# Optimization experiments

Measured on AMD Instinct MI355X. Metric: run time of the kernel, lower is better.

## Reference

```python
import jax, jax.numpy as jnp
import numpy as np

D_MODEL = 256
N_HEAD = 8
HEAD_DIM = D_MODEL // N_HEAD
N_TOTAL = 24576
B, T = 64, 512


def setup_inputs() -> dict:
    key = jax.random.key(0)
    ks = jax.random.split(key, 12)
    s = 1.0 / np.sqrt(D_MODEL)
    return {
        "x": jax.random.normal(ks[0], (N_TOTAL, D_MODEL), jnp.float32),
        "Wq": jax.random.uniform(ks[1], (D_MODEL, D_MODEL), jnp.float32, -s, s),
        "bq": jax.random.uniform(ks[2], (D_MODEL,), jnp.float32, -s, s),
        "Wk": jax.random.uniform(ks[3], (D_MODEL, D_MODEL), jnp.float32, -s, s),
        "bk": jax.random.uniform(ks[4], (D_MODEL,), jnp.float32, -s, s),
        "Wv": jax.random.uniform(ks[5], (D_MODEL, D_MODEL), jnp.float32, -s, s),
        "bv": jax.random.uniform(ks[6], (D_MODEL,), jnp.float32, -s, s),
        "Wp": jax.random.uniform(ks[7], (D_MODEL, D_MODEL), jnp.float32, -s, s),
        "bp": jax.random.uniform(ks[8], (D_MODEL,), jnp.float32, -s, s),
        "padpack_index": jax.random.randint(ks[9], (B, T), 0, N_TOTAL, jnp.int64 if jax.config.jax_enable_x64 else jnp.int32),
        "padpack_batch": jax.random.randint(ks[10], (B, T), 0, B, jnp.int32),
        "padpack_inverse_index": jax.random.randint(ks[11], (N_TOTAL,), 0, B * T, jnp.int64 if jax.config.jax_enable_x64 else jnp.int32),
    }


def reference(x, Wq, bq, Wk, bk, Wv, bv, Wp, bp, padpack_index, padpack_batch, padpack_inverse_index):
    # gather ragged tokens into packed [B, T, C]
    xp = x[padpack_index]
    # mask: True where packed slots share the same segment id (matches
    # original masked_fill(batch_i == batch_j, -1e9))
    mask = padpack_batch[:, :, None] == padpack_batch[:, None, :]  # [B,T,T]
    # QKV projections (torch Linear: x @ W.T + b), split heads
    def heads(w, b):
        h = xp @ w.T + b
        return h.reshape(B, T, N_HEAD, HEAD_DIM).transpose(0, 2, 1, 3)  # [B,H,T,D]
    q, k, v = heads(Wq, bq), heads(Wk, bk), heads(Wv, bv)
    att = jnp.einsum("bhtd,bhsd->bhts", q, k) * (1.0 / np.sqrt(HEAD_DIM))
    att = jnp.where(mask[:, None], jnp.float32(-1e9), att)
    att = jax.nn.softmax(att, axis=-1)
    y = jnp.einsum("bhts,bhsd->bhtd", att, v)  # [B,H,T,D]
    y = y.transpose(0, 2, 1, 3).reshape(B, T, D_MODEL)
    y = y @ Wp.T + bp
    # scatter back to ragged layout
    return y.reshape(B * T, D_MODEL)[padpack_inverse_index]
```

## Files before the change

kernel.cpp:

```cpp
#include <hip/hip_runtime.h>


typedef __attribute__((ext_vector_type(8))) short short8;
typedef __attribute__((ext_vector_type(4))) float f32x4;

#define N_TOTAL 24576
#define B_ 64
#define T_ 512
#define M_TOK 32768
#define DM 256
#define NH 8
#define HD 32

#define QSCALE 0.25503463f

__device__ __forceinline__ unsigned short f2bf(float f) {
  unsigned int u = __float_as_uint(f);
  u += 0x7fffu + ((u >> 16) & 1u);
  return (unsigned short)(u >> 16);
}

__global__ __launch_bounds__(256) void pack_kernel(
    const float* __restrict__ x, const float* __restrict__ Wq,
    const float* __restrict__ Wk, const float* __restrict__ Wv,
    const float* __restrict__ Wp, const float* __restrict__ bq,
    const float* __restrict__ bk, const float* __restrict__ bv,
    const int* __restrict__ idx,
    short* __restrict__ XP, short* __restrict__ WCAT, short* __restrict__ WPb,
    float* __restrict__ BCAT) {
  int gid = blockIdx.x * 256 + threadIdx.x;
  if (gid < 768)
    BCAT[gid] = (gid < 256) ? bq[gid] : (gid < 512 ? bk[gid - 256] : bv[gid - 512]);
  const float* src;
  short* dst;
  if (gid < 1048576) {
    int row = gid >> 5, seg = gid & 31;
    src = x + (size_t)idx[row] * DM + seg * 8;
    dst = XP + (size_t)gid * 8;
  } else if (gid < 1073152) {
    int u = gid - 1048576;
    int f = u >> 5, seg = u & 31;
    const float* W = (f < 256) ? Wq : ((f < 512) ? Wk : Wv);
    src = W + (size_t)(f & 255) * DM + seg * 8;
    dst = WCAT + (size_t)u * 8;
  } else {
    int u = gid - 1073152;
    src = Wp + (size_t)u * 8;
    dst = WPb + (size_t)u * 8;
  }
  const float4* s4 = (const float4*)src;
  float4 a = s4[0], b = s4[1];
  short8 o;
  o[0] = (short)f2bf(a.x); o[1] = (short)f2bf(a.y);
  o[2] = (short)f2bf(a.z); o[3] = (short)f2bf(a.w);
  o[4] = (short)f2bf(b.x); o[5] = (short)f2bf(b.y);
  o[6] = (short)f2bf(b.z); o[7] = (short)f2bf(b.w);
  *(short8*)dst = o;
}

__global__ __launch_bounds__(256) void qkv_gemm(
    const short* __restrict__ XP, const short* __restrict__ WCAT,
    const float* __restrict__ BCAT,
    unsigned short* __restrict__ Qb, unsigned short* __restrict__ Kb,
    unsigned short* __restrict__ Vt) {
  __shared__ __align__(16) short As[128 * 40];
  __shared__ __align__(16) short Bs[128 * 40];
  int tid = threadIdx.x;
  int lane = tid & 63, w = tid >> 6;
  int i = lane & 15, q = lane >> 4;
  int m0 = blockIdx.x * 128, n0 = blockIdx.y * 128;
  int wm = (w & 1) * 64, wn = (w >> 1) * 64;

  f32x4 zf = {0.f, 0.f, 0.f, 0.f};
  f32x4 acc[4][4];
#pragma unroll
  for (int mt = 0; mt < 4; mt++)
#pragma unroll
    for (int nt = 0; nt < 4; nt++) acc[mt][nt] = zf;

  for (int k0 = 0; k0 < 256; k0 += 32) {
#pragma unroll
    for (int p = 0; p < 2; ++p) {
      int u = tid + p * 256;
      int row = u >> 2, seg = u & 3;
      *(short8*)&As[row * 40 + seg * 8] =
          *(const short8*)&XP[(size_t)(m0 + row) * DM + k0 + seg * 8];
      *(short8*)&Bs[row * 40 + seg * 8] =
          *(const short8*)&WCAT[(size_t)(n0 + row) * DM + k0 + seg * 8];
    }
    __syncthreads();
    short8 a[4], bfr[4];
#pragma unroll
    for (int mt = 0; mt < 4; mt++)
      a[mt] = *(short8*)&As[(wm + mt * 16 + i) * 40 + q * 8];
#pragma unroll
    for (int nt = 0; nt < 4; nt++)
      bfr[nt] = *(short8*)&Bs[(wn + nt * 16 + i) * 40 + q * 8];
#pragma unroll
    for (int mt = 0; mt < 4; mt++)
#pragma unroll
      for (int nt = 0; nt < 4; nt++)
        acc[mt][nt] = __builtin_amdgcn_mfma_f32_16x16x32_bf16(a[mt], bfr[nt], acc[mt][nt], 0, 0, 0);
    __syncthreads();
  }

#pragma unroll
  for (int nt = 0; nt < 4; nt++) {
    int f = n0 + wn + nt * 16 + i;
    float bias = BCAT[f];
    int which = f >> 8;
    int fw = f & 255;
    int hh = fw >> 5, dd = fw & 31;
#pragma unroll
    for (int mt = 0; mt < 4; mt++) {
#pragma unroll
      for (int r = 0; r < 4; r++) {
        int token = m0 + wm + mt * 16 + q * 4 + r;
        int bb = token >> 9, tt = token & 511;
        int bh = bb * NH + hh;
        float val = acc[mt][nt][r] + bias;
        if (which == 0)
          Qb[((size_t)bh * T_ + tt) * HD + dd] = f2bf(val * QSCALE);
        else if (which == 1)
          Kb[((size_t)bh * T_ + tt) * HD + dd] = f2bf(val);
        else
          Vt[((size_t)bh * HD + dd) * T_ + tt] = f2bf(val);
      }
    }
  }
}

__global__ __launch_bounds__(256) void attn_kernel(
    const short* __restrict__ Qb, const short* __restrict__ Kb,
    const short* __restrict__ Vt, const int* __restrict__ batch,
    unsigned short* __restrict__ Y) {
  __shared__ __align__(16) short pscr[4][64 * 40];
  __shared__ int sbat[T_];
  int tid = threadIdx.x, w = tid >> 6, lane = tid & 63;
  int i = lane & 15, q = lane >> 4;
  int bx = blockIdx.x;
  int half = bx >> 9, bh = bx & 511;
  int b = bh >> 3, h = bh & 7;
  int t0 = half * 256 + w * 64;

  *(int2*)&sbat[tid * 2] = *(const int2*)&batch[b * T_ + tid * 2];
  __syncthreads();

  const short* Kbase = Kb + (size_t)bh * T_ * HD;
  const short* Vbase = Vt + (size_t)bh * HD * T_;
  short* pw = &pscr[w][0];

  short8 qf[4];
  unsigned int btpk[4];
#pragma unroll
  for (int mt = 0; mt < 4; mt++) {
    qf[mt] = *(const short8*)&Kbase[((size_t)(t0 + mt * 16 + i) - (size_t)T_ * HD * 0) * HD + q * 8];
  }
#pragma unroll
  for (int mt = 0; mt < 4; mt++)
    qf[mt] = *(const short8*)&Qb[((size_t)bh * T_ + t0 + mt * 16 + i) * HD + q * 8];
#pragma unroll
  for (int mt = 0; mt < 4; mt++) {
    int4 t4 = *(int4*)&sbat[t0 + mt * 16 + q * 4];
    btpk[mt] = (unsigned)t4.x | ((unsigned)t4.y << 8) | ((unsigned)t4.z << 16) |
               ((unsigned)t4.w << 24);
  }

  unsigned short ob = (i == 0) ? (unsigned short)0x3F80 : (unsigned short)0;
  short8 ones = {(short)ob, (short)ob, (short)ob, (short)ob,
                 (short)ob, (short)ob, (short)ob, (short)ob};

  f32x4 zf = {0.f, 0.f, 0.f, 0.f};
  f32x4 o[4][2], lacc[4];
#pragma unroll
  for (int mt = 0; mt < 4; mt++) {
    o[mt][0] = zf; o[mt][1] = zf; lacc[mt] = zf;
  }

  for (int s0 = 0; s0 < T_; s0 += 32) {
    short8 k0f = *(const short8*)&Kbase[(s0 + i) * HD + q * 8];
    short8 k1f = *(const short8*)&Kbase[(s0 + 16 + i) * HD + q * 8];
    short8 v0f = *(const short8*)&Vbase[(size_t)i * T_ + s0 + q * 8];
    short8 v1f = *(const short8*)&Vbase[(size_t)(16 + i) * T_ + s0 + q * 8];
    int bs0 = sbat[s0 + i];
    int bs1 = sbat[s0 + 16 + i];
#pragma unroll
    for (int mt = 0; mt < 4; mt++) {
      f32x4 st0 = __builtin_amdgcn_mfma_f32_16x16x32_bf16(qf[mt], k0f, zf, 0, 0, 0);
      f32x4 st1 = __builtin_amdgcn_mfma_f32_16x16x32_bf16(qf[mt], k1f, zf, 0, 0, 0);
#pragma unroll
      for (int r = 0; r < 4; r++) {
        int btv = (int)((btpk[mt] >> (8 * r)) & 0xffu);
        float e0 = __builtin_amdgcn_exp2f(st0[r]);
        float e1 = __builtin_amdgcn_exp2f(st1[r]);
        unsigned short p0 =
            (btv == bs0) ? (unsigned short)0 : (unsigned short)(__float_as_uint(e0) >> 16);
        unsigned short p1 =
            (btv == bs1) ? (unsigned short)0 : (unsigned short)(__float_as_uint(e1) >> 16);
        pw[(mt * 16 + q * 4 + r) * 40 + i] = (short)p0;
        pw[(mt * 16 + q * 4 + r) * 40 + 16 + i] = (short)p1;
      }
    }
#pragma unroll
    for (int mt = 0; mt < 4; mt++) {
      short8 pa = *(short8*)&pw[(mt * 16 + i) * 40 + q * 8];
      o[mt][0] = __builtin_amdgcn_mfma_f32_16x16x32_bf16(pa, v0f, o[mt][0], 0, 0, 0);
      o[mt][1] = __builtin_amdgcn_mfma_f32_16x16x32_bf16(pa, v1f, o[mt][1], 0, 0, 0);
      lacc[mt] = __builtin_amdgcn_mfma_f32_16x16x32_bf16(pa, ones, lacc[mt], 0, 0, 0);
    }
  }

#pragma unroll
  for (int mt = 0; mt < 4; mt++) {
#pragma unroll
    for (int r = 0; r < 4; r++) {
      float lv = __shfl(lacc[mt][r], lane & 48, 64);
      float inv = __builtin_amdgcn_rcpf(lv);
      size_t yb = ((size_t)b * T_ + t0 + mt * 16 + q * 4 + r) * DM + h * HD;
      Y[yb + i] = f2bf(o[mt][0][r] * inv);
      Y[yb + 16 + i] = f2bf(o[mt][1][r] * inv);
    }
  }
}

__global__ __launch_bounds__(256) void out_gemm(
    const short* __restrict__ Y, const short* __restrict__ WPb,
    const float* __restrict__ bp, const int* __restrict__ inv,
    float* __restrict__ out) {
  __shared__ __align__(16) short As[128 * 40];
  __shared__ __align__(16) short Bs[128 * 40];
  int tid = threadIdx.x;
  int lane = tid & 63, w = tid >> 6;
  int i = lane & 15, q = lane >> 4;
  int m0 = blockIdx.x * 128, n0 = blockIdx.y * 128;
  int wm = (w & 1) * 64, wn = (w >> 1) * 64;

  int iv0 = inv[m0 + (tid >> 2)];
  int iv1 = inv[m0 + (tid >> 2) + 64];

  f32x4 zf = {0.f, 0.f, 0.f, 0.f};
  f32x4 acc[4][4];
#pragma unroll
  for (int mt = 0; mt < 4; mt++)
#pragma unroll
    for (int nt = 0; nt < 4; nt++) acc[mt][nt] = zf;

  for (int k0 = 0; k0 < 256; k0 += 32) {
#pragma unroll
    for (int p = 0; p < 2; ++p) {
      int u = tid + p * 256;
      int row = u >> 2, seg = u & 3;
      int iv = p ? iv1 : iv0;
      *(short8*)&As[row * 40 + seg * 8] =
          *(const short8*)&Y[(size_t)iv * DM + k0 + seg * 8];
      *(short8*)&Bs[row * 40 + seg * 8] =
          *(const short8*)&WPb[(size_t)(n0 + row) * DM + k0 + seg * 8];
    }
    __syncthreads();
    short8 a[4], bfr[4];
#pragma unroll
    for (int mt = 0; mt < 4; mt++)
      a[mt] = *(short8*)&As[(wm + mt * 16 + i) * 40 + q * 8];
#pragma unroll
    for (int nt = 0; nt < 4; nt++)
      bfr[nt] = *(short8*)&Bs[(wn + nt * 16 + i) * 40 + q * 8];
#pragma unroll
    for (int mt = 0; mt < 4; mt++)
#pragma unroll
      for (int nt = 0; nt < 4; nt++)
        acc[mt][nt] = __builtin_amdgcn_mfma_f32_16x16x32_bf16(a[mt], bfr[nt], acc[mt][nt], 0, 0, 0);
    __syncthreads();
  }

#pragma unroll
  for (int nt = 0; nt < 4; nt++) {
    int f = n0 + wn + nt * 16 + i;
    float bias = bp[f];
#pragma unroll
    for (int mt = 0; mt < 4; mt++) {
#pragma unroll
      for (int r = 0; r < 4; r++) {
        int row = m0 + wm + mt * 16 + q * 4 + r;
        out[(size_t)row * DM + f] = acc[mt][nt][r] + bias;
      }
    }
  }
}

extern "C" void kernel_launch(void* const* d_in, const int* in_sizes, int n_in,
                              void* d_out, int out_size, void* d_ws, size_t ws_size,
                              hipStream_t stream) {
  const float* x = (const float*)d_in[0];
  const float* Wq = (const float*)d_in[1];
  const float* bq = (const float*)d_in[2];
  const float* Wk = (const float*)d_in[3];
  const float* bk = (const float*)d_in[4];
  const float* Wv = (const float*)d_in[5];
  const float* bv = (const float*)d_in[6];
  const float* Wp = (const float*)d_in[7];
  const float* bp = (const float*)d_in[8];
  const int* idx = (const int*)d_in[9];
  const int* batch = (const int*)d_in[10];
  const int* inv = (const int*)d_in[11];
  float* out = (float*)d_out;

  char* ws = (char*)d_ws;
  short* XP = (short*)(ws + 0);
  short* WCAT = (short*)(ws + 16777216);
  short* WPb = (short*)(ws + 17170432);
  float* BCAT = (float*)(ws + 17301504);
  unsigned short* Qb = (unsigned short*)(ws + 17304576);
  unsigned short* Kb = (unsigned short*)(ws + 34081792);
  unsigned short* Vt = (unsigned short*)(ws + 50859008);
  unsigned short* Yb = (unsigned short*)(ws + 67636224);

  pack_kernel<<<4224, 256, 0, stream>>>(x, Wq, Wk, Wv, Wp, bq, bk, bv, idx,
                                        XP, WCAT, WPb, BCAT);
  qkv_gemm<<<dim3(256, 6), 256, 0, stream>>>(XP, WCAT, BCAT, Qb, Kb, Vt);
  attn_kernel<<<1024, 256, 0, stream>>>((const short*)Qb, (const short*)Kb,
                                        (const short*)Vt, batch, Yb);
  out_gemm<<<dim3(192, 2), 256, 0, stream>>>((const short*)Yb, WPb, bp, inv, out);
}
```

Before: 195.0 us.

## Pipeline GEMM tile loads with triple-buffered direct global-to-LDS copies

Both the QKV and output GEMMs now stage A and B tiles straight from global memory into LDS with global_load_lds, using three buffers and a prefetch distance of two k-steps. This replaces the register round-trip and the double __syncthreads per iteration with explicit waitcnt plus barrier, so loads overlap the MFMA work. The LDS layout drops the padding in favour of an XOR swizzle to avoid bank conflicts. A redundant K load in attention is also removed. The cost is more LDS per block, which may lower occupancy, and correctness depends on the hand-tuned vmcnt values.

```diff
diff --git a/kernel.cpp b/kernel.cpp
--- a/kernel.cpp
+++ b/kernel.cpp
@@ -18,6 +18,12 @@
   unsigned int u = __float_as_uint(f);
   u += 0x7fffu + ((u >> 16) & 1u);
   return (unsigned short)(u >> 16);
+}
+
+__device__ __forceinline__ void gl_lds16(const void* g, void* l) {
+  __builtin_amdgcn_global_load_lds(
+      (const __attribute__((address_space(1))) unsigned int*)g,
+      (__attribute__((address_space(3))) unsigned int*)l, 16, 0, 0);
 }
 
 __global__ __launch_bounds__(256) void pack_kernel(
@@ -63,13 +69,13 @@
     const float* __restrict__ BCAT,
     unsigned short* __restrict__ Qb, unsigned short* __restrict__ Kb,
     unsigned short* __restrict__ Vt) {
-  __shared__ __align__(16) short As[128 * 40];
-  __shared__ __align__(16) short Bs[128 * 40];
+  __shared__ __align__(16) char smem[3 * 16384];
   int tid = threadIdx.x;
   int lane = tid & 63, w = tid >> 6;
   int i = lane & 15, q = lane >> 4;
   int m0 = blockIdx.x * 128, n0 = blockIdx.y * 128;
   int wm = (w & 1) * 64, wn = (w >> 1) * 64;
+  int csa = q ^ ((i >> 1) & 3);
 
   f32x4 zf = {0.f, 0.f, 0.f, 0.f};
   f32x4 acc[4][4];
@@ -78,30 +84,42 @@
 #pragma unroll
     for (int nt = 0; nt < 4; nt++) acc[mt][nt] = zf;
 
-  for (int k0 = 0; k0 < 256; k0 += 32) {
-#pragma unroll
-    for (int p = 0; p < 2; ++p) {
-      int u = tid + p * 256;
-      int row = u >> 2, seg = u & 3;
-      *(short8*)&As[row * 40 + seg * 8] =
-          *(const short8*)&XP[(size_t)(m0 + row) * DM + k0 + seg * 8];
-      *(short8*)&Bs[row * 40 + seg * 8] =
-          *(const short8*)&WCAT[(size_t)(n0 + row) * DM + k0 + seg * 8];
-    }
-    __syncthreads();
+  auto stage = [&](int k, int s) {
+#pragma unroll
+    for (int p = 0; p < 2; p++) {
+      int U = p * 256 + tid;
+      int row = U >> 2, c = U & 3;
+      int cs = c ^ ((row >> 1) & 3);
+      gl_lds16(XP + (size_t)(m0 + row) * DM + k * 32 + cs * 8,
+               smem + s * 16384 + U * 16);
+      gl_lds16(WCAT + (size_t)(n0 + row) * DM + k * 32 + cs * 8,
+               smem + s * 16384 + 8192 + U * 16);
+    }
+  };
+
+  stage(0, 0);
+  stage(1, 1);
+#pragma unroll
+  for (int k = 0; k < 8; k++) {
+    if (k == 7)
+      asm volatile("s_waitcnt vmcnt(0) lgkmcnt(0)\ns_barrier" ::: "memory");
+    else
+      asm volatile("s_waitcnt vmcnt(4) lgkmcnt(0)\ns_barrier" ::: "memory");
+    const short* Asb = (const short*)(smem + (k % 3) * 16384);
+    const short* Bsb = Asb + 8192 / 2;
     short8 a[4], bfr[4];
 #pragma unroll
     for (int mt = 0; mt < 4; mt++)
-      a[mt] = *(short8*)&As[(wm + mt * 16 + i) * 40 + q * 8];
+      a[mt] = *(const short8*)&Asb[(wm + mt * 16 + i) * 32 + csa * 8];
 #pragma unroll
     for (int nt = 0; nt < 4; nt++)
-      bfr[nt] = *(short8*)&Bs[(wn + nt * 16 + i) * 40 + q * 8];
+      bfr[nt] = *(const short8*)&Bsb[(wn + nt * 16 + i) * 32 + csa * 8];
+    if (k < 6) stage(k + 2, (k + 2) % 3);
 #pragma unroll
     for (int mt = 0; mt < 4; mt++)
 #pragma unroll
       for (int nt = 0; nt < 4; nt++)
         acc[mt][nt] = __builtin_amdgcn_mfma_f32_16x16x32_bf16(a[mt], bfr[nt], acc[mt][nt], 0, 0, 0);
-    __syncthreads();
   }
 
 #pragma unroll
@@ -153,10 +171,6 @@
   short8 qf[4];
   unsigned int btpk[4];
 #pragma unroll
-  for (int mt = 0; mt < 4; mt++) {
-    qf[mt] = *(const short8*)&Kbase[((size_t)(t0 + mt * 16 + i) - (size_t)T_ * HD * 0) * HD + q * 8];
-  }
-#pragma unroll
   for (int mt = 0; mt < 4; mt++)
     qf[mt] = *(const short8*)&Qb[((size_t)bh * T_ + t0 + mt * 16 + i) * HD + q * 8];
 #pragma unroll
@@ -227,16 +241,16 @@
     const short* __restrict__ Y, const short* __restrict__ WPb,
     const float* __restrict__ bp, const int* __restrict__ inv,
     float* __restrict__ out) {
-  __shared__ __align__(16) short As[128 * 40];
-  __shared__ __align__(16) short Bs[128 * 40];
+  __shared__ __align__(16) char smem[3 * 16384];
   int tid = threadIdx.x;
   int lane = tid & 63, w = tid >> 6;
   int i = lane & 15, q = lane >> 4;
   int m0 = blockIdx.x * 128, n0 = blockIdx.y * 128;
   int wm = (w & 1) * 64, wn = (w >> 1) * 64;
+  int csa = q ^ ((i >> 1) & 3);
 
   int iv0 = inv[m0 + (tid >> 2)];
-  int iv1 = inv[m0 + (tid >> 2) + 64];
+  int iv1 = inv[m0 + 64 + (tid >> 2)];
 
   f32x4 zf = {0.f, 0.f, 0.f, 0.f};
   f32x4 acc[4][4];
@@ -245,31 +259,42 @@
 #pragma unroll
     for (int nt = 0; nt < 4; nt++) acc[mt][nt] = zf;
 
-  for (int k0 = 0; k0 < 256; k0 += 32) {
-#pragma unroll
-    for (int p = 0; p < 2; ++p) {
-      int u = tid + p * 256;
-      int row = u >> 2, seg = u & 3;
+  auto stage = [&](int k, int s) {
+#pragma unroll
+    for (int p = 0; p < 2; p++) {
+      int U = p * 256 + tid;
+      int row = U >> 2, c = U & 3;
+      int cs = c ^ ((row >> 1) & 3);
       int iv = p ? iv1 : iv0;
-      *(short8*)&As[row * 40 + seg * 8] =
-          *(const short8*)&Y[(size_t)iv * DM + k0 + seg * 8];
-      *(short8*)&Bs[row * 40 + seg * 8] =
-          *(const short8*)&WPb[(size_t)(n0 + row) * DM + k0 + seg * 8];
-    }
-    __syncthreads();
+      gl_lds16(Y + (size_t)iv * DM + k * 32 + cs * 8, smem + s * 16384 + U * 16);
+      gl_lds16(WPb + (size_t)(n0 + row) * DM + k * 32 + cs * 8,
+               smem + s * 16384 + 8192 + U * 16);
+    }
+  };
+
+  stage(0, 0);
+  stage(1, 1);
+#pragma unroll
+  for (int k = 0; k < 8; k++) {
+    if (k == 7)
+      asm volatile("s_waitcnt vmcnt(0) lgkmcnt(0)\ns_barrier" ::: "memory");
+    else
+      asm volatile("s_waitcnt vmcnt(4) lgkmcnt(0)\ns_barrier" ::: "memory");
+    const short* Asb = (const short*)(smem + (k % 3) * 16384);
+    const short* Bsb = Asb + 8192 / 2;
     short8 a[4], bfr[4];
 #pragma unroll
     for (int mt = 0; mt < 4; mt++)
-      a[mt] = *(short8*)&As[(wm + mt * 16 + i) * 40 + q * 8];
+      a[mt] = *(const short8*)&Asb[(wm + mt * 16 + i) * 32 + csa * 8];
 #pragma unroll
     for (int nt = 0; nt < 4; nt++)
-      bfr[nt] = *(short8*)&Bs[(wn + nt * 16 + i) * 40 + q * 8];
+      bfr[nt] = *(const short8*)&Bsb[(wn + nt * 16 + i) * 32 + csa * 8];
+    if (k < 6) stage(k + 2, (k + 2) % 3);
 #pragma unroll
     for (int mt = 0; mt < 4; mt++)
 #pragma unroll
       for (int nt = 0; nt < 4; nt++)
         acc[mt][nt] = __builtin_amdgcn_mfma_f32_16x16x32_bf16(a[mt], bfr[nt], acc[mt][nt], 0, 0, 0);
-    __syncthreads();
   }
 
 #pragma unroll
```

Result: no change. 191.9 us (-1.6%).
